# Performance work log

Hardware: AMD Instinct MI355X
Metric: run time of the kernel (lower is better)

The kernel has to match this reference:

```python
import jax, jax.numpy as jnp
import numpy as np

B, T, C = 16, 2048, 256
TT = T  # maxlen
LAYER_ID, N_LAYER = 3, 6


def setup_inputs() -> dict:
    key = jax.random.key(0)
    ks = jax.random.split(key, 6)
    ratio_0_to_1 = LAYER_ID / (N_LAYER - 1)
    ratio_1_to_almost0 = 1.0 - LAYER_ID / N_LAYER

    h = np.arange(TT, dtype=np.float32)
    decay_speed = -5.0 + 8.0 * (h / (TT - 1)) ** (0.7 + 1.3 * ratio_0_to_1)
    curve = -(TT - 1 - h)  # curve[i] = -(maxlen-1-i)
    # Faithful init ww = exp(curve * decay_speed); clip exponent so the table
    # stays finite (raw init overflows to inf for large maxlen; time_w is a
    # learned parameter, so finite plausible values are appropriate).
    time_w = jnp.asarray(np.exp(np.clip(curve * decay_speed, -30.0, 0.0)), dtype=jnp.float32)

    i = np.arange(C, dtype=np.float32) / C  # x[0,0,i] = i / hidden_units
    time_mix_k = jnp.asarray((i ** ratio_1_to_almost0).reshape(1, 1, C), dtype=jnp.float32)
    time_mix_v = jnp.asarray((i ** ratio_1_to_almost0 + 0.3 * ratio_0_to_1).reshape(1, 1, C), dtype=jnp.float32)
    time_mix_r = jnp.asarray((i ** (0.5 * ratio_1_to_almost0)).reshape(1, 1, C), dtype=jnp.float32)

    x = jax.random.normal(ks[0], (B, T, C), dtype=jnp.float32)
    scale = 0.02
    Wk = scale * jax.random.normal(ks[1], (C, C), dtype=jnp.float32)
    Wv = scale * jax.random.normal(ks[2], (C, C), dtype=jnp.float32)
    Wr = scale * jax.random.normal(ks[3], (C, C), dtype=jnp.float32)
    Wo = scale * jax.random.normal(ks[4], (C, C), dtype=jnp.float32)
    return {"x": x, "time_w": time_w, "time_mix_k": time_mix_k,
            "time_mix_v": time_mix_v, "time_mix_r": time_mix_r,
            "Wk": Wk, "Wv": Wv, "Wr": Wr, "Wo": Wo}


def reference(x, time_w, time_mix_k, time_mix_v, time_mix_r, Wk, Wv, Wr, Wo):
    Bx, Tx, Cx = x.shape
    maxlen = time_w.shape[0]
    # time_shift: shift sequence right by one, zero-pad the first step
    xx = jnp.pad(x, ((0, 0), (1, 0), (0, 0)))[:, :-1]
    xk = x * time_mix_k + xx * (1.0 - time_mix_k)
    xv = x * time_mix_v + xx * (1.0 - time_mix_v)
    xr = x * time_mix_r + xx * (1.0 - time_mix_r)

    k = jnp.exp(jnp.clip(xk @ Wk, -60.0, 30.0))  # [B,T,C]
    v = xv @ Wv
    r = xr @ Wr

    sum_k = jnp.cumsum(k, axis=1)
    kv = k * v

    # Toeplitz decay matrix: W[t,u] = time_w[maxlen-1-(t-u)] for u<=t, else 0
    t_idx = jnp.arange(Tx)
    d = t_idx[:, None] - t_idx[None, :]  # lag t-u
    W = jnp.where(d >= 0, time_w[jnp.clip(maxlen - 1 - d, 0, maxlen - 1)], 0.0)

    wkv = jnp.einsum('tu,buc->btc', W, kv)  # O(T^2 * C) WKV mixing
    rwkv = jax.nn.sigmoid(r) * wkv / sum_k
    return rwkv @ Wo
```

## Files before the change

kernel.cpp:

```cpp
#include <hip/hip_runtime.h>
#include <hip/hip_bf16.h>

#define NB 16
#define NT 2048
#define NC 256
#define NM (NB*NT)
#define NCH 16
#define NCL (NT/NCH)

typedef __attribute__((ext_vector_type(8))) short short8;
typedef __attribute__((ext_vector_type(4))) short short4v;
typedef __attribute__((ext_vector_type(4))) unsigned short ushort4v;
typedef __attribute__((ext_vector_type(4))) float f32x4;

__device__ __forceinline__ unsigned short f2bf(float x){
    union { float f; unsigned u; } v; v.f = x;
    unsigned r = v.u + 0x7FFFu + ((v.u >> 16) & 1u);
    return (unsigned short)(r >> 16);
}
__device__ __forceinline__ float bf2f(unsigned short x){
    union { unsigned u; float f; } v; v.u = ((unsigned)x) << 16;
    return v.f;
}
__device__ __forceinline__ void gload16(const unsigned short* g, unsigned short* l){
    __builtin_amdgcn_global_load_lds((const __attribute__((address_space(1))) void*)g,
                                     (__attribute__((address_space(3))) void*)l, 16, 0, 0);
}


__global__ void prep_kernel(const float* __restrict__ tw,
                            const float* __restrict__ Wk, const float* __restrict__ Wv,
                            const float* __restrict__ Wr, const float* __restrict__ Wo,
                            unsigned short* __restrict__ WkT, unsigned short* __restrict__ WvT,
                            unsigned short* __restrict__ WrT, unsigned short* __restrict__ WoT,
                            unsigned short* __restrict__ Aexp){
    int gid = blockIdx.x*256 + threadIdx.x;
    {
        int n = gid >> 8, u = gid & 255;
        int usw = (u & ~63) | ((((u>>3)&7) ^ (n&7)) << 3) | (u & 7);
        int src = u*NC + n;
        WkT[n*NC + usw] = f2bf(Wk[src]);
        WvT[n*NC + usw] = f2bf(Wv[src]);
        WrT[n*NC + usw] = f2bf(Wr[src]);
        WoT[n*NC + usw] = f2bf(Wo[src]);
    }
    if (gid < 32768){
        int Di = gid >> 10, rem = gid & 1023;
        int r = rem >> 3, ql = rem & 7;
        int qlog = ql ^ (r & 7);
        int D = Di*64 - 1920;
        short8 vv;
        #pragma unroll
        for (int j = 0; j < 8; j++){
            int idx = 2047 + D - r + qlog*8 + j;
            float val = (idx >= 0 && idx < NT) ? tw[idx] : 0.f;
            vv[j] = (short)f2bf(val);
        }
        *(short8*)&Aexp[(size_t)gid*8] = vv;
    }
}

__global__ void mix_kernel(const float* __restrict__ x,
                           const float* __restrict__ tmk, const float* __restrict__ tmv,
                           const float* __restrict__ tmr,
                           unsigned short* __restrict__ xk, unsigned short* __restrict__ xv,
                           unsigned short* __restrict__ xr){
    int gid = blockIdx.x*256 + threadIdx.x;
    int m = gid >> 5;
    int c0 = (gid & 31) << 3;
    int t = m & (NT-1);
    size_t base = (size_t)m*NC + c0;
    float xa[8], xb[8];
    #pragma unroll
    for (int j=0;j<8;j+=4) *(float4*)&xa[j] = *(const float4*)&x[base+j];
    if (t > 0) {
        #pragma unroll
        for (int j=0;j<8;j+=4) *(float4*)&xb[j] = *(const float4*)&x[base - NC + j];
    } else {
        #pragma unroll
        for (int j=0;j<8;j++) xb[j]=0.f;
    }
    short8 ok, ov, orr;
    #pragma unroll
    for (int j=0;j<8;j++){
        float mk = tmk[c0+j], mv = tmv[c0+j], mr = tmr[c0+j];
        ok[j]  = (short)f2bf(xa[j]*mk + xb[j]*(1.f-mk));
        ov[j]  = (short)f2bf(xa[j]*mv + xb[j]*(1.f-mv));
        orr[j] = (short)f2bf(xa[j]*mr + xb[j]*(1.f-mr));
    }
    int csw = (c0 & ~63) | ((((c0>>3)&7) ^ (m&7)) << 3);
    size_t dst = (size_t)m*NC + csw;
    *(short8*)&xk[dst] = ok;
    *(short8*)&xv[dst] = ov;
    *(short8*)&xr[dst] = orr;
}

template<int MODE>
__global__ __launch_bounds__(256) void gemm_c(const unsigned short* __restrict__ A,
                                              const unsigned short* __restrict__ BT,
                                              void* __restrict__ outp,
                                              const unsigned short* __restrict__ vbT,
                                              unsigned short* __restrict__ kvt){
    __shared__ unsigned short smem[32768];
    unsigned short* As0 = smem;
    unsigned short* Bs0 = smem + 16384;
    const int tid = threadIdx.x;
    const int lane = tid & 63, w = tid >> 6;
    const int wm = (w >> 1) * 64, wn = (w & 1) * 64;
    const int m0 = blockIdx.x * 128, n0 = blockIdx.y * 128;
    const int lrow = lane & 15, kgrp = lane >> 4, lx = lane & 7;
    const int qrow = tid >> 3, qc = tid & 7;

    f32x4 acc[4][4] = {};

    auto STAGE = [&](int buf, int k0){
        #pragma unroll
        for (int i=0;i<4;i++){
            int row = qrow + 32*i;
            int q = row*8 + qc;
            gload16(A  + (size_t)(m0+row)*NC + k0 + qc*8, As0 + buf*8192 + q*8);
            gload16(BT + (size_t)(n0+row)*NC + k0 + qc*8, Bs0 + buf*8192 + q*8);
        }
    };

    STAGE(0, 0);
    __syncthreads();
    for (int s = 0; s < 4; ++s){
        if (s < 3) STAGE((s+1)&1, (s+1)*64);
        const unsigned short* as = As0 + (s&1)*8192;
        const unsigned short* bs = Bs0 + (s&1)*8192;
        #pragma unroll
        for (int ks = 0; ks < 2; ++ks){
            const int lk = ks*4 + kgrp;
            const int ch = (lk ^ lx) << 3;
            short8 a[4], b[4];
            #pragma unroll
            for (int mi=0;mi<4;mi++) a[mi] = *(const short8*)&as[(wm + mi*16 + lrow)*64 + ch];
            #pragma unroll
            for (int ni=0;ni<4;ni++) b[ni] = *(const short8*)&bs[(wn + ni*16 + lrow)*64 + ch];
            #pragma unroll
            for (int mi=0;mi<4;mi++)
            #pragma unroll
            for (int ni=0;ni<4;ni++)
                acc[mi][ni] = __builtin_amdgcn_mfma_f32_16x16x32_bf16(a[mi], b[ni], acc[mi][ni], 0,0,0);
        }
        __syncthreads();
    }

    const int orow = wm + kgrp*4;
    const int ocol = wn + lrow;
    if (MODE == 0 || MODE == 3){
        #pragma unroll
        for (int mi=0;mi<4;mi++)
        #pragma unroll
        for (int ni=0;ni<4;ni++)
        #pragma unroll
        for (int i=0;i<4;i++){
            float vv = acc[mi][ni][i];
            size_t off = (size_t)(m0 + orow + mi*16 + i)*NC + n0 + ocol + ni*16;
            if (MODE == 0) ((float*)outp)[off] = vv;
            if (MODE == 3) ((unsigned short*)outp)[off] = f2bf(1.f/(1.f+__expf(-vv)));
        }
    } else {
        const int b = m0 >> 11, t0b = m0 & 2047;
        unsigned short (*tileT)[136] = (unsigned short (*)[136])smem;
        #pragma unroll
        for (int mi=0;mi<4;mi++)
        #pragma unroll
        for (int ni=0;ni<4;ni++){
            const int cL = ocol + ni*16;
            const int t4 = orow + mi*16;
            short4v pk;
            if (MODE == 5){
                ushort4v v4 = *(const ushort4v*)&vbT[((size_t)(b*NC + n0 + cL))*NT + t0b + t4];
                #pragma unroll
                for (int i=0;i<4;i++){
                    float ke = __expf(fminf(fmaxf(acc[mi][ni][i],-60.f),30.f));
                    ((float*)outp)[(size_t)(m0 + t4 + i)*NC + n0 + cL] = ke;
                    pk[i] = (short)f2bf(ke * bf2f(v4[i]));
                }
            } else {
                #pragma unroll
                for (int i=0;i<4;i++) pk[i] = (short)f2bf(acc[mi][ni][i]);
            }
            *(short4v*)&tileT[cL][t4] = pk;
        }
        __syncthreads();
        #pragma unroll
        for (int p=0;p<8;p++){
            int c = (tid >> 4) + p*16;
            int t8 = (tid & 15) * 8;
            short8 vv = *(const short8*)&tileT[c][t8];
            if (MODE == 4){
                *(short8*)&((unsigned short*)outp)[((size_t)(b*NC + n0 + c))*NT + t0b + t8] = vv;
            } else {
                int row = n0 + c;
                int colp = (t8 & ~63) | ((((t8>>3)&7) ^ (row&7)) << 3);
                *(short8*)&kvt[((size_t)(b*NC + row))*NT + t0b + colp] = vv;
            }
        }
    }
}

__global__ void scan1(const float* __restrict__ kf, float* __restrict__ part){
    int gid = blockIdx.x*256 + threadIdx.x;
    int c = gid & 255, ch = (gid >> 8) & 15, b = gid >> 12;
    const float* p = kf + ((size_t)b*NT + ch*NCL)*NC + c;
    float s = 0.f;
    for (int i=0;i<NCL;i++) s += p[(size_t)i*NC];
    part[gid] = s;
}
__global__ void scan2(const float* __restrict__ kf, const float* __restrict__ part,
                      float* __restrict__ sumk){
    int gid = blockIdx.x*256 + threadIdx.x;
    int c = gid & 255, ch = (gid >> 8) & 15, b = gid >> 12;
    float off = 0.f;
    for (int j=0;j<ch;j++) off += part[((b*NCH + j)<<8) + c];
    const float* p = kf + ((size_t)b*NT + ch*NCL)*NC + c;
    float* o = sumk + ((size_t)b*NT + ch*NCL)*NC + c;
    float s = off;
    for (int i=0;i<NCL;i++){ s += p[(size_t)i*NC]; o[(size_t)i*NC] = s; }
}

__global__ __launch_bounds__(256) void gemm_wkv(const unsigned short* __restrict__ Aexp,
                                                const unsigned short* __restrict__ kvt,
                                                const unsigned short* __restrict__ srb,
                                                const float* __restrict__ sumk,
                                                unsigned short* __restrict__ rout){
    __shared__ unsigned short As[2][128*64];
    __shared__ unsigned short Bs[2][64*64];
    const int tid = threadIdx.x;
    const int lane = tid & 63, w = tid >> 6;
    const int wm = (w >> 1) * 64, wn = (w & 1) * 32;
    const int lrow = lane & 15, kgrp = lane >> 4, lx = lane & 7;
    const int qrow = tid >> 3, qc = tid & 7;

    const int id = blockIdx.x;
    const int j = id & 511, hi = id >> 9;
    const int t_idx = hi ? 15 - (j >> 5) : (j >> 5);
    const int combo = (j & 31) | (hi << 5);
    const int b  = combo >> 2;
    const int c0 = (combo & 3) * 64;
    const int t0 = t_idx * 128;
    const int nsteps = 2*t_idx + 2;
    const unsigned short* Ab = Aexp + (size_t)(30 - 2*t_idx)*8192;

    f32x4 acc[4][2] = {};

    auto STAGE = [&](int buf, int s){
        const int u0 = s*64;
        #pragma unroll
        for (int i=0;i<4;i++){
            int row = qrow + 32*i;
            gload16(Ab + (size_t)s*8192 + (size_t)(row*8+qc)*8, &As[buf][(row*8+qc)*8]);
        }
        #pragma unroll
        for (int i=0;i<2;i++){
            int row = qrow + 32*i;
            gload16(kvt + ((size_t)(b*NC + c0 + row))*NT + u0 + qc*8, &Bs[buf][(row*8+qc)*8]);
        }
    };

    STAGE(0, 0);
    __syncthreads();
    for (int s = 0; s < nsteps; ++s){
        if (s+1 < nsteps) STAGE((s+1)&1, s+1);
        const unsigned short* as = As[s&1];
        const unsigned short* bs = Bs[s&1];
        #pragma unroll
        for (int ks = 0; ks < 2; ++ks){
            const int lk = ks*4 + kgrp;
            const int ch = (lk ^ lx) << 3;
            short8 a[4], b8[2];
            #pragma unroll
            for (int mi=0;mi<4;mi++) a[mi]  = *(const short8*)&as[(wm + mi*16 + lrow)*64 + ch];
            #pragma unroll
            for (int ni=0;ni<2;ni++) b8[ni] = *(const short8*)&bs[(wn + ni*16 + lrow)*64 + ch];
            #pragma unroll
            for (int mi=0;mi<4;mi++)
            #pragma unroll
            for (int ni=0;ni<2;ni++)
                acc[mi][ni] = __builtin_amdgcn_mfma_f32_16x16x32_bf16(a[mi], b8[ni], acc[mi][ni], 0,0,0);
        }
        __syncthreads();
    }

    const int orow = wm + kgrp*4;
    const int ocol = c0 + wn + lrow;
    #pragma unroll
    for (int mi=0;mi<4;mi++)
    #pragma unroll
    for (int ni=0;ni<2;ni++)
    #pragma unroll
    for (int i=0;i<4;i++){
        int t = t0 + orow + mi*16 + i;
        int col = ocol + ni*16;
        size_t g = (size_t)(b*NT + t)*NC + col;
        float sr = bf2f(srb[g]);
        float sk = sumk[g];
        float vv = sr * acc[mi][ni][i] / sk;
        int csw = (col & ~63) | ((((col>>3)&7) ^ (t&7)) << 3) | (col & 7);
        rout[(size_t)(b*NT + t)*NC + csw] = f2bf(vv);
    }
}

extern "C" void kernel_launch(void* const* d_in, const int* in_sizes, int n_in,
                              void* d_out, int out_size, void* d_ws, size_t ws_size,
                              hipStream_t stream) {
    const float* x   = (const float*)d_in[0];
    const float* tw  = (const float*)d_in[1];
    const float* tmk = (const float*)d_in[2];
    const float* tmv = (const float*)d_in[3];
    const float* tmr = (const float*)d_in[4];
    const float* Wk  = (const float*)d_in[5];
    const float* Wv  = (const float*)d_in[6];
    const float* Wr  = (const float*)d_in[7];
    const float* Wo  = (const float*)d_in[8];

    char* ws = (char*)d_ws;
    const size_t MC = (size_t)NM*NC;
    unsigned short* xk   = (unsigned short*)(ws);
    unsigned short* xv   = (unsigned short*)(ws + MC*2);
    unsigned short* xr   = (unsigned short*)(ws + MC*4);
    float*          kf   = (float*)(ws + MC*6);
    unsigned short* vbT  = (unsigned short*)(ws + MC*10);
    unsigned short* srb  = (unsigned short*)(ws + MC*12);
    float*          sumk = (float*)(ws + MC*14);
    unsigned short* kvt  = (unsigned short*)(ws + MC*18);
    unsigned short* Aexp = (unsigned short*)(ws + MC*20);
    unsigned short* WkT  = (unsigned short*)(ws + MC*20 + 524288);
    unsigned short* WvT  = WkT + NC*NC;
    unsigned short* WrT  = WvT + NC*NC;
    unsigned short* WoT  = WrT + NC*NC;
    float*          part = (float*)(ws + MC*20 + 1048576);
    unsigned short* rwkvb = xk;

    prep_kernel<<<256,256,0,stream>>>(tw, Wk,Wv,Wr,Wo, WkT,WvT,WrT,WoT, Aexp);
    mix_kernel<<<(int)(MC/8/256),256,0,stream>>>(x,tmk,tmv,tmr,xk,xv,xr);
    gemm_c<4><<<dim3(NM/128,NC/128),256,0,stream>>>(xv,WvT,vbT,nullptr,nullptr);
    gemm_c<5><<<dim3(NM/128,NC/128),256,0,stream>>>(xk,WkT,kf,vbT,kvt);
    gemm_c<3><<<dim3(NM/128,NC/128),256,0,stream>>>(xr,WrT,srb,nullptr,nullptr);
    scan1<<<256,256,0,stream>>>(kf,part);
    scan2<<<256,256,0,stream>>>(kf,part,sumk);
    gemm_wkv<<<1024,256,0,stream>>>(Aexp,kvt,srb,sumk,rwkvb);
    gemm_c<0><<<dim3(NM/128,NC/128),256,0,stream>>>(rwkvb,WoT,(float*)d_out,nullptr,nullptr);
}
```

Measured before the change: 138.9 us.

## Read Toeplitz A tiles directly from global and widen K step to 128

The WKV GEMM no longer stages the precomputed Toeplitz decay tiles (Aexp) through LDS. Each lane now loads its A fragments straight from global memory, which relies on the small table staying in cache, and the Aexp precompute drops its XOR swizzle to match. The K step doubles to 128, so half as many barriers are needed, and only the kv tile is double-buffered in LDS with a new swizzle. The trade-off is more global/L2 traffic on the A side and possible load latency exposed at each MFMA, in exchange for less LDS use and fewer synchronisations.

```diff
diff --git a/kernel.cpp b/kernel.cpp
--- a/kernel.cpp
+++ b/kernel.cpp
@@ -47,12 +47,11 @@
     if (gid < 32768){
         int Di = gid >> 10, rem = gid & 1023;
         int r = rem >> 3, ql = rem & 7;
-        int qlog = ql ^ (r & 7);
         int D = Di*64 - 1920;
         short8 vv;
         #pragma unroll
         for (int j = 0; j < 8; j++){
-            int idx = 2047 + D - r + qlog*8 + j;
+            int idx = 2047 + D - r + ql*8 + j;
             float val = (idx >= 0 && idx < NT) ? tw[idx] : 0.f;
             vv[j] = (short)f2bf(val);
         }
@@ -227,13 +226,11 @@
                                                 const unsigned short* __restrict__ srb,
                                                 const float* __restrict__ sumk,
                                                 unsigned short* __restrict__ rout){
-    __shared__ unsigned short As[2][128*64];
-    __shared__ unsigned short Bs[2][64*64];
+    __shared__ unsigned short Bs[2][64*128];
     const int tid = threadIdx.x;
     const int lane = tid & 63, w = tid >> 6;
     const int wm = (w >> 1) * 64, wn = (w & 1) * 32;
-    const int lrow = lane & 15, kgrp = lane >> 4, lx = lane & 7;
-    const int qrow = tid >> 3, qc = tid & 7;
+    const int lrow = lane & 15, kgrp = lane >> 4;
 
     const int id = blockIdx.x;
     const int j = id & 511, hi = id >> 9;
@@ -242,22 +239,18 @@
     const int b  = combo >> 2;
     const int c0 = (combo & 3) * 64;
     const int t0 = t_idx * 128;
-    const int nsteps = 2*t_idx + 2;
+    const int nsteps = t_idx + 1;
     const unsigned short* Ab = Aexp + (size_t)(30 - 2*t_idx)*8192;
 
     f32x4 acc[4][2] = {};
 
     auto STAGE = [&](int buf, int s){
-        const int u0 = s*64;
+        const int u0 = s*128;
         #pragma unroll
         for (int i=0;i<4;i++){
-            int row = qrow + 32*i;
-            gload16(Ab + (size_t)s*8192 + (size_t)(row*8+qc)*8, &As[buf][(row*8+qc)*8]);
-        }
-        #pragma unroll
-        for (int i=0;i<2;i++){
-            int row = qrow + 32*i;
-            gload16(kvt + ((size_t)(b*NC + c0 + row))*NT + u0 + qc*8, &Bs[buf][(row*8+qc)*8]);
+            int idx = (w*4 + i)*64 + lane;
+            int row = idx >> 4, cp = idx & 15;
+            gload16(kvt + ((size_t)(b*NC + c0 + row))*NT + u0 + cp*8, &Bs[buf][0] + (size_t)idx*8);
         }
     };
 
@@ -265,17 +258,19 @@
     __syncthreads();
     for (int s = 0; s < nsteps; ++s){
         if (s+1 < nsteps) STAGE((s+1)&1, s+1);
-        const unsigned short* as = As[s&1];
-        const unsigned short* bs = Bs[s&1];
-        #pragma unroll
-        for (int ks = 0; ks < 2; ++ks){
-            const int lk = ks*4 + kgrp;
-            const int ch = (lk ^ lx) << 3;
+        const unsigned short* bs = &Bs[s&1][0];
+        const unsigned short* ap = Ab + (size_t)s*16384;
+        #pragma unroll
+        for (int ks = 0; ks < 4; ++ks){
+            const int kc = ks*4 + kgrp;
             short8 a[4], b8[2];
             #pragma unroll
-            for (int mi=0;mi<4;mi++) a[mi]  = *(const short8*)&as[(wm + mi*16 + lrow)*64 + ch];
-            #pragma unroll
-            for (int ni=0;ni<2;ni++) b8[ni] = *(const short8*)&bs[(wn + ni*16 + lrow)*64 + ch];
+            for (int mi=0;mi<4;mi++)
+                a[mi] = *(const short8*)&ap[(size_t)(kc>>3)*8192 + (wm + mi*16 + lrow)*64 + (kc&7)*8];
+            const int cph = ((kc & 8) | ((kc & 7) ^ (lrow & 7))) << 3;
+            #pragma unroll
+            for (int ni=0;ni<2;ni++)
+                b8[ni] = *(const short8*)&bs[(wn + ni*16 + lrow)*128 + cph];
             #pragma unroll
             for (int mi=0;mi<4;mi++)
             #pragma unroll
```

Measured after the change: 169.8 us. +22.2%, slower.
